# Performance work log

Hardware: AMD Instinct MI355X
Metric: run time of the kernel (lower is better)

The kernel has to match this reference:

```python
import jax, jax.numpy as jnp
import numpy as np

N_NODES = 100000
N_EDGES = 1600000
DROP_P = 0.5  # F.dropout default, training=True by default in the source
LRELU_SLOPE = 0.01
EPS = 1e-12


def setup_inputs() -> dict:
    key = jax.random.key(0)
    ks = jax.random.split(key, 8)
    x = jax.random.normal(ks[0], (N_NODES, 64), dtype=jnp.float32)
    edge_index = jax.random.randint(ks[1], (2, N_EDGES), 0, N_NODES, dtype=jnp.int64)
    s = 1.0 / np.sqrt(64)
    W1_l = jax.random.uniform(ks[2], (64, 32), jnp.float32, -s, s)
    W1_r = jax.random.uniform(ks[3], (64, 32), jnp.float32, -s, s)
    b1 = jnp.zeros((32,), jnp.float32)
    s2 = 1.0 / np.sqrt(32)
    W2_l = jax.random.uniform(ks[4], (32, 64), jnp.float32, -s2, s2)
    W2_r = jax.random.uniform(ks[5], (32, 64), jnp.float32, -s2, s2)
    b2 = jnp.zeros((64,), jnp.float32)
    return {"x": x, "edge_index": edge_index, "W1_l": W1_l, "b1": b1,
            "W1_r": W1_r, "W2_l": W2_l, "b2": b2, "W2_r": W2_r}


def _sage_conv(x, src, dst, W_l, b, W_r, n):
    # mean aggregation of source features onto destinations (PyG SAGEConv)
    msg = x[src]                                                 # [E, d]
    agg = jax.ops.segment_sum(msg, dst, num_segments=n)          # [N, d]
    cnt = jax.ops.segment_sum(jnp.ones((src.shape[0],), x.dtype), dst, num_segments=n)
    mean = agg / jnp.maximum(cnt, 1.0)[:, None]
    return mean @ W_l + b + x @ W_r


def _dropout(x, key):
    keep = jax.random.bernoulli(key, 1.0 - DROP_P, x.shape)
    return jnp.where(keep, x / (1.0 - DROP_P), 0.0).astype(x.dtype)


def reference(x, edge_index, W1_l, b1, W1_r, W2_l, b2, W2_r):
    n = x.shape[0]
    src, dst = edge_index[0], edge_index[1]
    dk = jax.random.split(jax.random.key(42), 2)
    h = _sage_conv(x, src, dst, W1_l, b1, W1_r, n)
    h = jax.nn.leaky_relu(h, LRELU_SLOPE)
    h = _dropout(h, dk[0])
    h = _sage_conv(h, src, dst, W2_l, b2, W2_r, n)
    h = _dropout(h, dk[1])
    norm = jnp.sqrt(jnp.sum(h * h, axis=1, keepdims=True))
    return h / jnp.maximum(norm, EPS)
```

## Files before the change

kernel.cpp:

```cpp
#include <hip/hip_runtime.h>

#define N_NODES 100000
#define N_EDGES 1600000
#define NPB 32
#define NB (N_NODES / NPB)
#define CAP 704
#define NCC 49
#define CAPA 34816
#define NFB 64
#define BPC 16

typedef float v2f __attribute__((ext_vector_type(2)));

struct U2 { unsigned a, b; };

__host__ __device__ constexpr U2 tf2x32(unsigned k0, unsigned k1, unsigned c0, unsigned c1) {
  unsigned ks2 = k0 ^ k1 ^ 0x1BD11BDAu;
  unsigned x0 = c0 + k0, x1 = c1 + k1;
#define TFR(r) { x0 += x1; x1 = (x1 << (r)) | (x1 >> (32 - (r))); x1 ^= x0; }
  TFR(13) TFR(15) TFR(26) TFR(6)
  x0 += k1;  x1 += ks2 + 1u;
  TFR(17) TFR(29) TFR(16) TFR(24)
  x0 += ks2; x1 += k0 + 2u;
  TFR(13) TFR(15) TFR(26) TFR(6)
  x0 += k0;  x1 += k1 + 3u;
  TFR(17) TFR(29) TFR(16) TFR(24)
  x0 += k1;  x1 += ks2 + 4u;
  TFR(13) TFR(15) TFR(26) TFR(6)
  x0 += ks2; x1 += k0 + 5u;
#undef TFR
  return U2{x0, x1};
}

constexpr U2 DK0 = tf2x32(0u, 42u, 0u, 0u);
constexpr U2 DK1 = tf2x32(0u, 42u, 0u, 1u);

__device__ __forceinline__ bool keep_bit(unsigned k0, unsigned k1, unsigned j) {
  U2 w = tf2x32(k0, k1, 0u, j);
  return ((w.a ^ w.b) >> 31) == 0u;
}

__device__ __forceinline__ unsigned short f2bf(float f) {
  unsigned u = __float_as_uint(f);
  u += 0x7FFFu + ((u >> 16) & 1u);
  return (unsigned short)(u >> 16);
}
__device__ __forceinline__ v2f up2(unsigned r) {
  v2f v;
  v.x = __uint_as_float(r << 16);
  v.y = __uint_as_float(r & 0xFFFF0000u);
  return v;
}

__global__ __launch_bounds__(256, 4) void k_transform1(
    const float* __restrict__ x, const float* __restrict__ Wl,
    const float* __restrict__ Wr, unsigned short* __restrict__ xlb,
    float* __restrict__ xr) {
  __shared__ __align__(16) float rv[4][64];
  int lane = threadIdx.x & 63;
  int wv = (threadIdx.x >> 6) & 3;
  const float* W = (lane < 32) ? Wl : Wr;
  int c = lane & 31;
  float w[64];
#pragma unroll
  for (int k = 0; k < 64; ++k) w[k] = W[k * 32 + c];
  int wid0 = (int)((blockIdx.x * blockDim.x + threadIdx.x) >> 6);
  int wstride = (int)((gridDim.x * blockDim.x) >> 6);
  for (int wid = wid0; wid < N_NODES; wid += wstride) {
    float xv = x[wid * 64 + lane];
    asm volatile("s_waitcnt lgkmcnt(0)" ::: "memory");
    rv[wv][lane] = xv;
    asm volatile("s_waitcnt lgkmcnt(0)" ::: "memory");
    v2f s0 = {0.f, 0.f}, s1 = {0.f, 0.f};
#pragma unroll
    for (int k = 0; k < 64; k += 4) {
      float4 r = *(const float4*)&rv[wv][k];
      v2f w0; w0.x = w[k + 0]; w0.y = w[k + 1];
      v2f w1; w1.x = w[k + 2]; w1.y = w[k + 3];
      v2f p0; p0.x = r.x; p0.y = r.y;
      v2f p1; p1.x = r.z; p1.y = r.w;
      s0 += p0 * w0;
      s1 += p1 * w1;
    }
    float s = (s0.x + s0.y) + (s1.x + s1.y);
    if (lane < 32) xlb[wid * 32 + c] = f2bf(s);
    else           xr[wid * 32 + c] = s;
  }
}

__global__ __launch_bounds__(256) void k_binA(
    const int* __restrict__ src, const int* __restrict__ dst,
    int* __restrict__ curA, unsigned* __restrict__ bufA) {
  __shared__ int hist[NCC];
  __shared__ int offsL[NCC + 1];
  __shared__ int baseL[NCC];
  __shared__ int place[NCC];
  __shared__ unsigned stag[2048];
  __shared__ unsigned char cellb[2048];
  int t = threadIdx.x;
  for (long long start = (long long)blockIdx.x * 2048; start < N_EDGES;
       start += (long long)gridDim.x * 2048) {
    int n = (int)min((long long)2048, (long long)N_EDGES - start);
    for (int i = t; i < NCC; i += 256) hist[i] = 0;
    __syncthreads();
    unsigned pv[8]; int pc[8];
#pragma unroll
    for (int i = 0; i < 8; ++i) {
      int idx = t + i * 256;
      if (idx < n) {
        int d = dst[start + idx];
        int s = src[start + idx];
        int cc = d >> 11;
        pc[i] = cc;
        pv[i] = (unsigned)s | ((unsigned)(d & 2047) << 17);
        atomicAdd(&hist[cc], 1);
      } else pc[i] = -1;
    }
    __syncthreads();
    if (t < 64) {
      int lane = t;
      int v = (lane < NCC) ? hist[lane] : 0;
      int x = v;
#pragma unroll
      for (int o = 1; o < 64; o <<= 1) {
        int y = __shfl_up(x, o, 64);
        if (lane >= o) x += y;
      }
      if (lane < NCC) {
        offsL[lane] = x - v;
        place[lane] = 0;
        if (v > 0) baseL[lane] = atomicAdd(&curA[lane], v);
      }
      if (lane == NCC - 1) offsL[NCC] = x;
    }
    __syncthreads();
#pragma unroll
    for (int i = 0; i < 8; ++i) {
      if (pc[i] >= 0) {
        int p = atomicAdd(&place[pc[i]], 1);
        int sl = offsL[pc[i]] + p;
        stag[sl] = pv[i];
        cellb[sl] = (unsigned char)pc[i];
      }
    }
    __syncthreads();
    for (int s2 = t; s2 < n; s2 += 256) {
      int cell = cellb[s2];
      int pos = baseL[cell] + (s2 - offsL[cell]);
      if (pos < CAPA) bufA[(size_t)cell * CAPA + pos] = stag[s2];
    }
    __syncthreads();
  }
}

__global__ __launch_bounds__(256) void k_binB(
    const unsigned* __restrict__ bufA, const int* __restrict__ curA,
    int* __restrict__ cur, unsigned* __restrict__ buf) {
  __shared__ int hist[NFB];
  __shared__ int offsL[NFB + 1];
  __shared__ int baseL[NFB];
  __shared__ int place[NFB];
  __shared__ unsigned stag[2048];
  __shared__ unsigned char cellb[2048];
  int cellc = blockIdx.x / BPC;
  int slice = blockIdx.x % BPC;
  int t = threadIdx.x;
  int cnt = min(curA[cellc], CAPA);
  const unsigned* in = bufA + (size_t)cellc * CAPA;
  for (int start = slice * 2048; start < cnt; start += BPC * 2048) {
    int n = min(2048, cnt - start);
    for (int i = t; i < NFB; i += 256) hist[i] = 0;
    __syncthreads();
    unsigned pv[8]; int pb[8];
#pragma unroll
    for (int i = 0; i < 8; ++i) {
      int idx = t + i * 256;
      if (idx < n) {
        unsigned w = in[start + idx];
        int dlow = (int)(w >> 17);
        int fb = dlow >> 5;
        pb[i] = fb;
        pv[i] = (w & 0x1FFFFu) | ((unsigned)(dlow & 31) << 17);
        atomicAdd(&hist[fb], 1);
      } else pb[i] = -1;
    }
    __syncthreads();
    if (t < 64) {
      int lane = t;
      int v = hist[lane];
      int x = v;
#pragma unroll
      for (int o = 1; o < 64; o <<= 1) {
        int y = __shfl_up(x, o, 64);
        if (lane >= o) x += y;
      }
      offsL[lane] = x - v;
      place[lane] = 0;
      if (v > 0) baseL[lane] = atomicAdd(&cur[cellc * NFB + lane], v);
      if (lane == 63) offsL[NFB] = x;
    }
    __syncthreads();
#pragma unroll
    for (int i = 0; i < 8; ++i) {
      if (pb[i] >= 0) {
        int p = atomicAdd(&place[pb[i]], 1);
        int sl = offsL[pb[i]] + p;
        stag[sl] = pv[i];
        cellb[sl] = (unsigned char)pb[i];
      }
    }
    __syncthreads();
    for (int s2 = t; s2 < n; s2 += 256) {
      int fb = cellb[s2];
      int pos = baseL[fb] + (s2 - offsL[fb]);
      if (pos < CAP) buf[(size_t)(cellc * NFB + fb) * CAP + pos] = stag[s2];
    }
    __syncthreads();
  }
}

__global__ __launch_bounds__(1024) void k_bscan(
    const int* __restrict__ cur, int* __restrict__ bbase) {
  __shared__ int warp_sums[16];
  __shared__ int s_running;
  int t = threadIdx.x;
  int lane = t & 63, w = t >> 6;
  if (t == 0) s_running = 0;
  __syncthreads();
  for (int base = 0; base < NB; base += 1024) {
    int i = base + t;
    int v = (i < NB) ? min(cur[i], CAP) : 0;
    int x = v;
#pragma unroll
    for (int o = 1; o < 64; o <<= 1) {
      int y = __shfl_up(x, o, 64);
      if (lane >= o) x += y;
    }
    if (lane == 63) warp_sums[w] = x;
    __syncthreads();
    if (w == 0) {
      int ws = (lane < 16) ? warp_sums[lane] : 0;
#pragma unroll
      for (int o = 1; o < 16; o <<= 1) {
        int y = __shfl_up(ws, o, 64);
        if (lane >= o) ws += y;
      }
      if (lane < 16) warp_sums[lane] = ws;
    }
    __syncthreads();
    int incl = x + (w > 0 ? warp_sums[w - 1] : 0);
    int excl = s_running + incl - v;
    if (i < NB) bbase[i] = excl;
    __syncthreads();
    if (t == 1023) s_running += incl;
    __syncthreads();
  }
}

__global__ __launch_bounds__(256) void k_bfill(
    const unsigned* __restrict__ buf, const int* __restrict__ cur,
    const int* __restrict__ bbase, int* __restrict__ deg,
    int* __restrict__ offs, int* __restrict__ eidx) {
  __shared__ int ncnt[NPB];
  __shared__ int ncur[NPB];
  __shared__ unsigned sbuf[CAP];
  int b = blockIdx.x, t = threadIdx.x;
  if (t < NPB) ncnt[t] = 0;
  __syncthreads();
  int nb = min(cur[b], CAP);
  const unsigned* bb = buf + (size_t)b * CAP;
  for (int slot = t; slot < nb; slot += 256) {
    unsigned w = bb[slot];
    sbuf[slot] = w;
    atomicAdd(&ncnt[w >> 17], 1);
  }
  __syncthreads();
  if (t < 64) {
    int lane = t;
    int c = (lane < NPB) ? ncnt[lane] : 0;
    int x = c;
#pragma unroll
    for (int o = 1; o < 32; o <<= 1) {
      int y = __shfl_up(x, o, 64);
      if (lane >= o) x += y;
    }
    if (lane < NPB) {
      int excl = x - c;
      ncur[lane] = excl;
      int gn = b * NPB + lane;
      deg[gn] = c;
      offs[gn] = bbase[b] + excl;
    }
  }
  __syncthreads();
  int base = bbase[b];
  for (int slot = t; slot < nb; slot += 256) {
    unsigned w = sbuf[slot];
    int p = atomicAdd(&ncur[w >> 17], 1);
    eidx[base + p] = (int)(w & 0x1FFFF);
  }
}

__global__ __launch_bounds__(256) void k_gather1(
    const unsigned short* __restrict__ xlb, const float* __restrict__ xr,
    const int* __restrict__ offs, const int* __restrict__ deg,
    const int* __restrict__ eidx, const float* __restrict__ b1,
    unsigned short* __restrict__ hpb) {
  int pair = (int)((blockIdx.x * blockDim.x + threadIdx.x) >> 6);
  int lane = threadIdx.x & 63;
  int half = lane >> 5;
  int node = pair * 2 + half;
  if (node >= N_NODES) return;
  int g = (lane >> 3) & 3;
  int ch = lane & 7;
  int c32 = lane & 31;
  int off = offs[node];
  int dg = deg[node];
  float xr_v = xr[node * 32 + c32];
  float b1_v = b1[c32];
  const uint2* x2 = (const uint2*)xlb;
  v2f acc01 = {0.f, 0.f}, acc23 = {0.f, 0.f};
  int k = 0;
  for (; k + 8 <= dg; k += 8) {
    int s0 = eidx[off + k + g];
    int s1 = eidx[off + k + 4 + g];
    uint2 r0 = x2[s0 * 8 + ch];
    uint2 r1 = x2[s1 * 8 + ch];
    acc01 += up2(r0.x); acc23 += up2(r0.y);
    acc01 += up2(r1.x); acc23 += up2(r1.y);
  }
  for (; k < dg; k += 4) {
    if (k + g < dg) {
      int s = eidx[off + k + g];
      uint2 r = x2[s * 8 + ch];
      acc01 += up2(r.x); acc23 += up2(r.y);
    }
  }
  float a0 = acc01.x, a1 = acc01.y, a2 = acc23.x, a3 = acc23.y;
  a0 += __shfl_xor(a0, 8, 64); a0 += __shfl_xor(a0, 16, 64);
  a1 += __shfl_xor(a1, 8, 64); a1 += __shfl_xor(a1, 16, 64);
  a2 += __shfl_xor(a2, 8, 64); a2 += __shfl_xor(a2, 16, 64);
  a3 += __shfl_xor(a3, 8, 64); a3 += __shfl_xor(a3, 16, 64);
  int chunk = c32 >> 2, sub = lane & 3;
  int srcl = (half << 5) + chunk;
  float t0 = __shfl(a0, srcl, 64);
  float t1 = __shfl(a1, srcl, 64);
  float t2 = __shfl(a2, srcl, 64);
  float t3 = __shfl(a3, srcl, 64);
  float val = (sub == 0) ? t0 : (sub == 1) ? t1 : (sub == 2) ? t2 : t3;
  float inv = 1.0f / fmaxf((float)dg, 1.0f);
  int j = node * 32 + c32;
  float v = val * inv + b1_v + xr_v;
  v = (v > 0.f) ? v : 0.01f * v;
  float h = keep_bit(DK0.a, DK0.b, (unsigned)j) ? 2.0f * v : 0.0f;
  hpb[j] = f2bf(h);
}

__global__ __launch_bounds__(256, 4) void k_out(
    const unsigned short* __restrict__ hpb, const int* __restrict__ offs,
    const int* __restrict__ deg, const int* __restrict__ eidx,
    const float* __restrict__ W2l, const float* __restrict__ b2,
    const float* __restrict__ W2r, float* __restrict__ out) {
  __shared__ __align__(16) float rv[4][64];
  int lane = threadIdx.x & 63;
  int wv = (threadIdx.x >> 6) & 3;
  int g = lane >> 3, ch = lane & 7;
  float wl[32], wr[32];
#pragma unroll
  for (int kk = 0; kk < 32; ++kk) {
    wl[kk] = W2l[kk * 64 + lane];
    wr[kk] = W2r[kk * 64 + lane];
  }
  float bias = b2[lane];
  const uint2* h2 = (const uint2*)hpb;
  int wid0 = (int)((blockIdx.x * blockDim.x + threadIdx.x) >> 6);
  int wstride = (int)((gridDim.x * blockDim.x) >> 6);
  for (int wid = wid0; wid < N_NODES; wid += wstride) {
    int off = offs[wid];
    int dg = deg[wid];
    uint2 own = h2[wid * 8 + ch];
    v2f acc01 = {0.f, 0.f}, acc23 = {0.f, 0.f};
    int k = 0;
    for (; k + 16 <= dg; k += 16) {
      int s0 = eidx[off + k + g];
      int s1 = eidx[off + k + 8 + g];
      uint2 r0 = h2[s0 * 8 + ch];
      uint2 r1 = h2[s1 * 8 + ch];
      acc01 += up2(r0.x); acc23 += up2(r0.y);
      acc01 += up2(r1.x); acc23 += up2(r1.y);
    }
    for (; k < dg; k += 8) {
      if (k + g < dg) {
        int s = eidx[off + k + g];
        uint2 r = h2[s * 8 + ch];
        acc01 += up2(r.x); acc23 += up2(r.y);
      }
    }
    float a0 = acc01.x, a1 = acc01.y, a2 = acc23.x, a3 = acc23.y;
    a0 += __shfl_xor(a0, 8, 64); a0 += __shfl_xor(a0, 16, 64); a0 += __shfl_xor(a0, 32, 64);
    a1 += __shfl_xor(a1, 8, 64); a1 += __shfl_xor(a1, 16, 64); a1 += __shfl_xor(a1, 32, 64);
    a2 += __shfl_xor(a2, 8, 64); a2 += __shfl_xor(a2, 16, 64); a2 += __shfl_xor(a2, 32, 64);
    a3 += __shfl_xor(a3, 8, 64); a3 += __shfl_xor(a3, 16, 64); a3 += __shfl_xor(a3, 32, 64);
    float inv = 1.0f / fmaxf((float)dg, 1.0f);
    asm volatile("s_waitcnt lgkmcnt(0)" ::: "memory");
    if (lane < 8) {
      float4 v;
      v.x = a0 * inv; v.y = a1 * inv; v.z = a2 * inv; v.w = a3 * inv;
      *(float4*)&rv[wv][lane * 4] = v;
    } else if (lane < 16) {
      float4 v;
      v.x = __uint_as_float(own.x << 16);
      v.y = __uint_as_float(own.x & 0xFFFF0000u);
      v.z = __uint_as_float(own.y << 16);
      v.w = __uint_as_float(own.y & 0xFFFF0000u);
      *(float4*)&rv[wv][32 + (lane - 8) * 4] = v;
    }
    asm volatile("s_waitcnt lgkmcnt(0)" ::: "memory");
    v2f sa = {0.f, 0.f}, sb = {0.f, 0.f};
#pragma unroll
    for (int kk = 0; kk < 32; kk += 4) {
      float4 r1 = *(const float4*)&rv[wv][kk];
      float4 r2 = *(const float4*)&rv[wv][32 + kk];
      v2f w0; w0.x = wl[kk + 0]; w0.y = wl[kk + 1];
      v2f w1; w1.x = wl[kk + 2]; w1.y = wl[kk + 3];
      v2f u0; u0.x = wr[kk + 0]; u0.y = wr[kk + 1];
      v2f u1; u1.x = wr[kk + 2]; u1.y = wr[kk + 3];
      v2f p0; p0.x = r1.x; p0.y = r1.y;
      v2f p1; p1.x = r1.z; p1.y = r1.w;
      v2f q0; q0.x = r2.x; q0.y = r2.y;
      v2f q1; q1.x = r2.z; q1.y = r2.w;
      sa += p0 * w0;  sa += p1 * w1;
      sb += q0 * u0;  sb += q1 * u1;
    }
    float v = (sa.x + sa.y) + (sb.x + sb.y) + bias;
    unsigned j = (unsigned)(wid * 64 + lane);
    float d = keep_bit(DK1.a, DK1.b, j) ? 2.0f * v : 0.0f;
    float ss = d * d;
#pragma unroll
    for (int o = 32; o > 0; o >>= 1) ss += __shfl_xor(ss, o, 64);
    float scale = 1.0f / fmaxf(sqrtf(ss), 1e-12f);
    out[j] = d * scale;
  }
}

extern "C" void kernel_launch(void* const* d_in, const int* in_sizes, int n_in,
                              void* d_out, int out_size, void* d_ws, size_t ws_size,
                              hipStream_t stream) {
  const float* x   = (const float*)d_in[0];
  const int*   ei  = (const int*)d_in[1];
  const float* W1l = (const float*)d_in[2];
  const float* b1  = (const float*)d_in[3];
  const float* W1r = (const float*)d_in[4];
  const float* W2l = (const float*)d_in[5];
  const float* b2  = (const float*)d_in[6];
  const float* W2r = (const float*)d_in[7];
  float* out = (float*)d_out;

  const int* src = ei;
  const int* dst = ei + N_EDGES;

  const size_t F32 = (size_t)N_NODES * 32;
  char* w = (char*)d_ws;
  unsigned* bufA = (unsigned*)w;
  float* xr      = (float*)w;
  w += F32 * sizeof(float);
  unsigned* buf  = (unsigned*)w;
  unsigned short* xlb = (unsigned short*)w;
  unsigned short* hpb = xlb + F32;
  w += F32 * 2 * sizeof(unsigned short);
  int* curA  = (int*)w; w += NCC * sizeof(int);
  int* cur   = (int*)w; w += NB * sizeof(int);
  int* bbase = (int*)w; w += NB * sizeof(int);
  int* deg   = (int*)w; w += N_NODES * sizeof(int);
  int* offs  = (int*)w; w += N_NODES * sizeof(int);
  int* eidx  = (int*)w;

  hipMemsetAsync(curA, 0, (size_t)(NCC + NB) * sizeof(int), stream);

  k_binA<<<(N_EDGES + 2047) / 2048, 256, 0, stream>>>(src, dst, curA, bufA);
  k_binB<<<NCC * BPC, 256, 0, stream>>>(bufA, curA, cur, buf);
  k_bscan<<<1, 1024, 0, stream>>>(cur, bbase);
  k_bfill<<<NB, 256, 0, stream>>>(buf, cur, bbase, deg, offs, eidx);

  k_transform1<<<1024, 256, 0, stream>>>(x, W1l, W1r, xlb, xr);
  k_gather1<<<(N_NODES / 2 + 3) / 4, 256, 0, stream>>>(xlb, xr, offs, deg, eidx, b1, hpb);
  k_out<<<1024, 256, 0, stream>>>(hpb, offs, deg, eidx, W2l, b2, W2r, out);
}
```

Baseline: 264.5 us.

## Split bf16 feature tables into column halves and separate layer-2 gather

Stores the 32-column bf16 node features as two 16-column half tables, and runs the gathers as two passes over nodes, one per half. Each pass reads a 3.2 MB table that fits in cache, so random neighbour reads should hit cache more often. Layer-2 aggregation moves out of the fused output kernel into its own gather kernel that writes fp32 means, which k_out2 then reads. This costs an extra launch, an extra fp32 round trip through memory, and a second read of the edge index list per pass.

```diff
diff --git a/kernel.cpp b/kernel.cpp
--- a/kernel.cpp
+++ b/kernel.cpp
@@ -9,6 +9,8 @@
 #define CAPA 34816
 #define NFB 64
 #define BPC 16
+#define N16 (N_NODES * 16)
+#define GHB 6250
 
 typedef float v2f __attribute__((ext_vector_type(2)));
 
@@ -54,7 +56,7 @@
 
 __global__ __launch_bounds__(256, 4) void k_transform1(
     const float* __restrict__ x, const float* __restrict__ Wl,
-    const float* __restrict__ Wr, unsigned short* __restrict__ xlb,
+    const float* __restrict__ Wr, unsigned short* __restrict__ xlbh,
     float* __restrict__ xr) {
   __shared__ __align__(16) float rv[4][64];
   int lane = threadIdx.x & 63;
@@ -83,7 +85,7 @@
       s1 += p1 * w1;
     }
     float s = (s0.x + s0.y) + (s1.x + s1.y);
-    if (lane < 32) xlb[wid * 32 + c] = f2bf(s);
+    if (lane < 32) xlbh[(size_t)(c >> 4) * N16 + wid * 16 + (c & 15)] = f2bf(s);
     else           xr[wid * 32 + c] = s;
   }
 }
@@ -302,69 +304,118 @@
 }
 
 __global__ __launch_bounds__(256) void k_gather1(
-    const unsigned short* __restrict__ xlb, const float* __restrict__ xr,
+    const unsigned short* __restrict__ xlbh, const float* __restrict__ xr,
     const int* __restrict__ offs, const int* __restrict__ deg,
     const int* __restrict__ eidx, const float* __restrict__ b1,
-    unsigned short* __restrict__ hpb) {
-  int pair = (int)((blockIdx.x * blockDim.x + threadIdx.x) >> 6);
-  int lane = threadIdx.x & 63;
-  int half = lane >> 5;
-  int node = pair * 2 + half;
-  if (node >= N_NODES) return;
-  int g = (lane >> 3) & 3;
-  int ch = lane & 7;
-  int c32 = lane & 31;
+    unsigned short* __restrict__ hpbh) {
+  int bb = blockIdx.x;
+  int G = 0, nb = bb;
+  if (nb >= GHB) { G = 1; nb -= GHB; }
+  int tid = threadIdx.x;
+  int lane = tid & 63;
+  int node = nb * 16 + (tid >> 4);
+  int g = (tid >> 2) & 3;
+  int ch = tid & 3;
+  int c = tid & 15;
+  int col = G * 16 + c;
   int off = offs[node];
   int dg = deg[node];
-  float xr_v = xr[node * 32 + c32];
-  float b1_v = b1[c32];
-  const uint2* x2 = (const uint2*)xlb;
+  float xr_v = xr[node * 32 + col];
+  float b1_v = b1[col];
+  const uint2* H = (const uint2*)(xlbh + (size_t)G * N16);
   v2f acc01 = {0.f, 0.f}, acc23 = {0.f, 0.f};
   int k = 0;
   for (; k + 8 <= dg; k += 8) {
     int s0 = eidx[off + k + g];
     int s1 = eidx[off + k + 4 + g];
-    uint2 r0 = x2[s0 * 8 + ch];
-    uint2 r1 = x2[s1 * 8 + ch];
+    uint2 r0 = H[s0 * 4 + ch];
+    uint2 r1 = H[s1 * 4 + ch];
     acc01 += up2(r0.x); acc23 += up2(r0.y);
     acc01 += up2(r1.x); acc23 += up2(r1.y);
   }
   for (; k < dg; k += 4) {
     if (k + g < dg) {
       int s = eidx[off + k + g];
-      uint2 r = x2[s * 8 + ch];
+      uint2 r = H[s * 4 + ch];
       acc01 += up2(r.x); acc23 += up2(r.y);
     }
   }
   float a0 = acc01.x, a1 = acc01.y, a2 = acc23.x, a3 = acc23.y;
-  a0 += __shfl_xor(a0, 8, 64); a0 += __shfl_xor(a0, 16, 64);
-  a1 += __shfl_xor(a1, 8, 64); a1 += __shfl_xor(a1, 16, 64);
-  a2 += __shfl_xor(a2, 8, 64); a2 += __shfl_xor(a2, 16, 64);
-  a3 += __shfl_xor(a3, 8, 64); a3 += __shfl_xor(a3, 16, 64);
-  int chunk = c32 >> 2, sub = lane & 3;
-  int srcl = (half << 5) + chunk;
+  a0 += __shfl_xor(a0, 4, 64); a0 += __shfl_xor(a0, 8, 64);
+  a1 += __shfl_xor(a1, 4, 64); a1 += __shfl_xor(a1, 8, 64);
+  a2 += __shfl_xor(a2, 4, 64); a2 += __shfl_xor(a2, 8, 64);
+  a3 += __shfl_xor(a3, 4, 64); a3 += __shfl_xor(a3, 8, 64);
+  int srcl = (lane & 48) + (c >> 2);
   float t0 = __shfl(a0, srcl, 64);
   float t1 = __shfl(a1, srcl, 64);
   float t2 = __shfl(a2, srcl, 64);
   float t3 = __shfl(a3, srcl, 64);
+  int sub = lane & 3;
   float val = (sub == 0) ? t0 : (sub == 1) ? t1 : (sub == 2) ? t2 : t3;
   float inv = 1.0f / fmaxf((float)dg, 1.0f);
-  int j = node * 32 + c32;
+  int j = node * 32 + col;
   float v = val * inv + b1_v + xr_v;
   v = (v > 0.f) ? v : 0.01f * v;
   float h = keep_bit(DK0.a, DK0.b, (unsigned)j) ? 2.0f * v : 0.0f;
-  hpb[j] = f2bf(h);
-}
-
-__global__ __launch_bounds__(256, 4) void k_out(
-    const unsigned short* __restrict__ hpb, const int* __restrict__ offs,
+  hpbh[(size_t)G * N16 + node * 16 + c] = f2bf(h);
+}
+
+__global__ __launch_bounds__(256) void k_gather2(
+    const unsigned short* __restrict__ hpbh, const int* __restrict__ offs,
     const int* __restrict__ deg, const int* __restrict__ eidx,
+    float* __restrict__ aggh) {
+  int bb = blockIdx.x;
+  int G = 0, nb = bb;
+  if (nb >= GHB) { G = 1; nb -= GHB; }
+  int tid = threadIdx.x;
+  int lane = tid & 63;
+  int node = nb * 16 + (tid >> 4);
+  int g = (tid >> 2) & 3;
+  int ch = tid & 3;
+  int c = tid & 15;
+  int off = offs[node];
+  int dg = deg[node];
+  const uint2* H = (const uint2*)(hpbh + (size_t)G * N16);
+  v2f acc01 = {0.f, 0.f}, acc23 = {0.f, 0.f};
+  int k = 0;
+  for (; k + 8 <= dg; k += 8) {
+    int s0 = eidx[off + k + g];
+    int s1 = eidx[off + k + 4 + g];
+    uint2 r0 = H[s0 * 4 + ch];
+    uint2 r1 = H[s1 * 4 + ch];
+    acc01 += up2(r0.x); acc23 += up2(r0.y);
+    acc01 += up2(r1.x); acc23 += up2(r1.y);
+  }
+  for (; k < dg; k += 4) {
+    if (k + g < dg) {
+      int s = eidx[off + k + g];
+      uint2 r = H[s * 4 + ch];
+      acc01 += up2(r.x); acc23 += up2(r.y);
+    }
+  }
+  float a0 = acc01.x, a1 = acc01.y, a2 = acc23.x, a3 = acc23.y;
+  a0 += __shfl_xor(a0, 4, 64); a0 += __shfl_xor(a0, 8, 64);
+  a1 += __shfl_xor(a1, 4, 64); a1 += __shfl_xor(a1, 8, 64);
+  a2 += __shfl_xor(a2, 4, 64); a2 += __shfl_xor(a2, 8, 64);
+  a3 += __shfl_xor(a3, 4, 64); a3 += __shfl_xor(a3, 8, 64);
+  int srcl = (lane & 48) + (c >> 2);
+  float t0 = __shfl(a0, srcl, 64);
+  float t1 = __shfl(a1, srcl, 64);
+  float t2 = __shfl(a2, srcl, 64);
+  float t3 = __shfl(a3, srcl, 64);
+  int sub = lane & 3;
+  float val = (sub == 0) ? t0 : (sub == 1) ? t1 : (sub == 2) ? t2 : t3;
+  float inv = 1.0f / fmaxf((float)dg, 1.0f);
+  aggh[(size_t)G * N16 + node * 16 + c] = val * inv;
+}
+
+__global__ __launch_bounds__(256, 4) void k_out2(
+    const unsigned short* __restrict__ hpbh, const float* __restrict__ aggh,
     const float* __restrict__ W2l, const float* __restrict__ b2,
     const float* __restrict__ W2r, float* __restrict__ out) {
   __shared__ __align__(16) float rv[4][64];
   int lane = threadIdx.x & 63;
   int wv = (threadIdx.x >> 6) & 3;
-  int g = lane >> 3, ch = lane & 7;
   float wl[32], wr[32];
 #pragma unroll
   for (int kk = 0; kk < 32; ++kk) {
@@ -372,47 +423,22 @@
     wr[kk] = W2r[kk * 64 + lane];
   }
   float bias = b2[lane];
-  const uint2* h2 = (const uint2*)hpb;
   int wid0 = (int)((blockIdx.x * blockDim.x + threadIdx.x) >> 6);
   int wstride = (int)((gridDim.x * blockDim.x) >> 6);
   for (int wid = wid0; wid < N_NODES; wid += wstride) {
-    int off = offs[wid];
-    int dg = deg[wid];
-    uint2 own = h2[wid * 8 + ch];
-    v2f acc01 = {0.f, 0.f}, acc23 = {0.f, 0.f};
-    int k = 0;
-    for (; k + 16 <= dg; k += 16) {
-      int s0 = eidx[off + k + g];
-      int s1 = eidx[off + k + 8 + g];
-      uint2 r0 = h2[s0 * 8 + ch];
-      uint2 r1 = h2[s1 * 8 + ch];
-      acc01 += up2(r0.x); acc23 += up2(r0.y);
-      acc01 += up2(r1.x); acc23 += up2(r1.y);
-    }
-    for (; k < dg; k += 8) {
-      if (k + g < dg) {
-        int s = eidx[off + k + g];
-        uint2 r = h2[s * 8 + ch];
-        acc01 += up2(r.x); acc23 += up2(r.y);
-      }
-    }
-    float a0 = acc01.x, a1 = acc01.y, a2 = acc23.x, a3 = acc23.y;
-    a0 += __shfl_xor(a0, 8, 64); a0 += __shfl_xor(a0, 16, 64); a0 += __shfl_xor(a0, 32, 64);
-    a1 += __shfl_xor(a1, 8, 64); a1 += __shfl_xor(a1, 16, 64); a1 += __shfl_xor(a1, 32, 64);
-    a2 += __shfl_xor(a2, 8, 64); a2 += __shfl_xor(a2, 16, 64); a2 += __shfl_xor(a2, 32, 64);
-    a3 += __shfl_xor(a3, 8, 64); a3 += __shfl_xor(a3, 16, 64); a3 += __shfl_xor(a3, 32, 64);
-    float inv = 1.0f / fmaxf((float)dg, 1.0f);
     asm volatile("s_waitcnt lgkmcnt(0)" ::: "memory");
     if (lane < 8) {
-      float4 v;
-      v.x = a0 * inv; v.y = a1 * inv; v.z = a2 * inv; v.w = a3 * inv;
+      const float* ap = aggh + ((lane < 4) ? 0 : (size_t)N16) + wid * 16 + (lane & 3) * 4;
+      float4 v = *(const float4*)ap;
       *(float4*)&rv[wv][lane * 4] = v;
     } else if (lane < 16) {
+      const uint2* Hp = (const uint2*)(hpbh + ((lane < 12) ? 0 : (size_t)N16));
+      uint2 o = Hp[wid * 4 + (lane & 3)];
       float4 v;
-      v.x = __uint_as_float(own.x << 16);
-      v.y = __uint_as_float(own.x & 0xFFFF0000u);
-      v.z = __uint_as_float(own.y << 16);
-      v.w = __uint_as_float(own.y & 0xFFFF0000u);
+      v.x = __uint_as_float(o.x << 16);
+      v.y = __uint_as_float(o.x & 0xFFFF0000u);
+      v.z = __uint_as_float(o.y << 16);
+      v.w = __uint_as_float(o.y & 0xFFFF0000u);
       *(float4*)&rv[wv][32 + (lane - 8) * 4] = v;
     }
     asm volatile("s_waitcnt lgkmcnt(0)" ::: "memory");
@@ -463,10 +489,11 @@
   char* w = (char*)d_ws;
   unsigned* bufA = (unsigned*)w;
   float* xr      = (float*)w;
+  float* aggh    = (float*)w;
   w += F32 * sizeof(float);
   unsigned* buf  = (unsigned*)w;
-  unsigned short* xlb = (unsigned short*)w;
-  unsigned short* hpb = xlb + F32;
+  unsigned short* xlbh = (unsigned short*)w;
+  unsigned short* hpbh = xlbh + 2 * (size_t)N16;
   w += F32 * 2 * sizeof(unsigned short);
   int* curA  = (int*)w; w += NCC * sizeof(int);
   int* cur   = (int*)w; w += NB * sizeof(int);
@@ -482,7 +509,8 @@
   k_bscan<<<1, 1024, 0, stream>>>(cur, bbase);
   k_bfill<<<NB, 256, 0, stream>>>(buf, cur, bbase, deg, offs, eidx);
 
-  k_transform1<<<1024, 256, 0, stream>>>(x, W1l, W1r, xlb, xr);
-  k_gather1<<<(N_NODES / 2 + 3) / 4, 256, 0, stream>>>(xlb, xr, offs, deg, eidx, b1, hpb);
-  k_out<<<1024, 256, 0, stream>>>(hpb, offs, deg, eidx, W2l, b2, W2r, out);
-}
+  k_transform1<<<1024, 256, 0, stream>>>(x, W1l, W1r, xlbh, xr);
+  k_gather1<<<2 * GHB, 256, 0, stream>>>(xlbh, xr, offs, deg, eidx, b1, hpbh);
+  k_gather2<<<2 * GHB, 256, 0, stream>>>(hpbh, offs, deg, eidx, aggh);
+  k_out2<<<1024, 256, 0, stream>>>(hpbh, aggh, W2l, b2, W2r, out);
+}
```

After: 272.9 us. 1.03x slower.
